# Kernel tuning notes

Hardware: AMD Instinct MI355X
Metric: run time of the kernel (lower is better)

Reference implementation:

```python
import jax, jax.numpy as jnp
import numpy as np

NUM_HEADS = 16
D_MODEL = 1024
D_K = 64
D_V = 64
NEG_INF = -1e9


def setup_inputs() -> dict:
    key = jax.random.key(0)
    ks = jax.random.split(key, 7)
    B, S = 2, 2048
    Q = jax.random.normal(ks[0], (B, S, D_MODEL), dtype=jnp.float32)
    K = jax.random.normal(ks[1], (B, S, D_MODEL), dtype=jnp.float32)
    V = jax.random.normal(ks[2], (B, S, D_MODEL), dtype=jnp.float32)
    s = 1.0 / np.sqrt(D_MODEL)
    W_q = jax.random.normal(ks[3], (D_MODEL, D_K * NUM_HEADS), dtype=jnp.float32) * s
    W_k = jax.random.normal(ks[4], (D_MODEL, D_K), dtype=jnp.float32) * s
    W_v = jax.random.normal(ks[5], (D_MODEL, D_V), dtype=jnp.float32) * s
    W_o = jax.random.normal(ks[6], (D_V * NUM_HEADS, D_MODEL), dtype=jnp.float32) * (1.0 / np.sqrt(D_V * NUM_HEADS))
    return {"Q": Q, "K": K, "V": V, "W_q": W_q, "W_k": W_k, "W_v": W_v, "W_o": W_o}


def reference(Q, K, V, W_q, W_k, W_v, W_o):
    B, Sq, _ = Q.shape
    Sk = K.shape[1]
    # projections: Q -> per-head, K/V -> single shared head (MQA)
    q = (Q @ W_q).reshape(B, Sq, NUM_HEADS, D_K).transpose(0, 2, 1, 3)  # [B,H,Sq,Dk]
    k = K @ W_k  # [B,Sk,Dk]
    v = V @ W_v  # [B,Sk,Dv]
    scores = jnp.einsum('bhqd,bkd->bhqk', q, k) / jnp.sqrt(jnp.float32(D_K))
    causal = jnp.tril(jnp.ones((Sq, Sk), dtype=bool))  # [Sq,Sk]
    scores = jnp.where(causal[None, None], scores, NEG_INF)
    attn = jax.nn.softmax(scores, axis=-1)  # [B,H,Sq,Sk]
    out = jnp.einsum('bhqk,bkd->bhqd', attn, v)  # [B,H,Sq,Dv]
    out = out.transpose(0, 2, 1, 3).reshape(B, Sq, NUM_HEADS * D_V)
    return out @ W_o
```

## Files before the change

### kernel.cpp

```cpp
#include <hip/hip_runtime.h>
#include <hip/hip_bf16.h>
#include <cstdint>

typedef __bf16 bf16_t;
typedef __bf16 bf16x8 __attribute__((ext_vector_type(8)));
typedef __bf16 bf16x4 __attribute__((ext_vector_type(4)));
typedef float  floatx4 __attribute__((ext_vector_type(4)));

__device__ __forceinline__ bf16_t f2bf(float x) { return (bf16_t)x; }

__device__ __forceinline__ void gll16(const void* g, void* l) {
  __builtin_amdgcn_global_load_lds((const __attribute__((address_space(1))) void*)g,
                                   (__attribute__((address_space(3))) void*)l, 16, 0, 0);
}

#define S_LEN 2048
#define NHEAD 16
#define NTILE 32

__global__ __launch_bounds__(256) void transpose_w2(const float* __restrict__ W0,
                                                    const float* __restrict__ W1,
                                                    bf16_t* __restrict__ O0,
                                                    bf16_t* __restrict__ O1,
                                                    int K, int N) {
  const float* W = blockIdx.z ? W1 : W0;
  bf16_t* Wt = blockIdx.z ? O1 : O0;
  __shared__ float tile[32][33];
  int n0 = blockIdx.x * 32, k0 = blockIdx.y * 32;
  int tx = threadIdx.x & 31, ty = threadIdx.x >> 5;
#pragma unroll
  for (int r = 0; r < 4; ++r)
    tile[ty + 8 * r][tx] = W[(size_t)(k0 + ty + 8 * r) * N + n0 + tx];
  __syncthreads();
#pragma unroll
  for (int r = 0; r < 4; ++r)
    Wt[(size_t)(n0 + ty + 8 * r) * K + k0 + tx] = f2bf(tile[tx][ty + 8 * r]);
}

template <int OUTMODE, bool A_FP32>
__global__ __launch_bounds__(256, 2) void gemm_async(const void* __restrict__ Ain,
                                                     const bf16_t* __restrict__ Bt,
                                                     void* __restrict__ Cout,
                                                     int M, int N, int K) {
  constexpr int BK = 64;
  __shared__ __align__(16) bf16_t As[64 * BK];
  __shared__ __align__(16) bf16_t Bs[128 * BK];
  const int tid = threadIdx.x;
  const int wave = tid >> 6, lane = tid & 63;
  const int quad = lane >> 4, lm = lane & 15;
  const int wr = wave >> 1, wc = wave & 1;
  const int m0 = blockIdx.x * 64, n0 = blockIdx.y * 128;

  floatx4 acc[2][4];
#pragma unroll
  for (int i = 0; i < 2; ++i)
#pragma unroll
    for (int j = 0; j < 4; ++j) acc[i][j] = (floatx4){0.f, 0.f, 0.f, 0.f};

  for (int k0 = 0; k0 < K; k0 += BK) {
    if constexpr (A_FP32) {
#pragma unroll
      for (int rd = 0; rd < 2; ++rd) {
        int idx = rd * 256 + tid, row = idx >> 3, ch = (idx & 7) ^ (row & 7);
        const float* src = (const float*)Ain + (size_t)(m0 + row) * K + k0 + ch * 8;
        float4 f0 = *(const float4*)src;
        float4 f1 = *(const float4*)(src + 4);
        bf16x8 o;
        o[0] = f2bf(f0.x); o[1] = f2bf(f0.y); o[2] = f2bf(f0.z); o[3] = f2bf(f0.w);
        o[4] = f2bf(f1.x); o[5] = f2bf(f1.y); o[6] = f2bf(f1.z); o[7] = f2bf(f1.w);
        *(bf16x8*)&As[idx * 8] = o;
      }
    } else {
#pragma unroll
      for (int rd = 0; rd < 2; ++rd) {
        int idx = rd * 256 + tid, row = idx >> 3, ch = (idx & 7) ^ (row & 7);
        gll16((const bf16_t*)Ain + (size_t)(m0 + row) * K + k0 + ch * 8,
              As + (rd * 256 + wave * 64) * 8);
      }
    }
#pragma unroll
    for (int rd = 0; rd < 4; ++rd) {
      int idx = rd * 256 + tid, row = idx >> 3, ch = (idx & 7) ^ (row & 7);
      gll16(Bt + (size_t)(n0 + row) * K + k0 + ch * 8,
            Bs + (rd * 256 + wave * 64) * 8);
    }
    __syncthreads();
    const int sw = lm & 7;
    bf16x8 af[2][2], bfr[4][2];
#pragma unroll
    for (int i = 0; i < 2; ++i) {
      const bf16_t* base = &As[(wr * 32 + i * 16 + lm) * BK];
      af[i][0] = *(const bf16x8*)(base + ((quad ^ sw) * 8));
      af[i][1] = *(const bf16x8*)(base + (((4 + quad) ^ sw) * 8));
    }
#pragma unroll
    for (int j = 0; j < 4; ++j) {
      const bf16_t* base = &Bs[(wc * 64 + j * 16 + lm) * BK];
      bfr[j][0] = *(const bf16x8*)(base + ((quad ^ sw) * 8));
      bfr[j][1] = *(const bf16x8*)(base + (((4 + quad) ^ sw) * 8));
    }
#pragma unroll
    for (int ks = 0; ks < 2; ++ks)
#pragma unroll
      for (int i = 0; i < 2; ++i)
#pragma unroll
        for (int j = 0; j < 4; ++j)
          acc[i][j] = __builtin_amdgcn_mfma_f32_16x16x32_bf16(af[i][ks], bfr[j][ks],
                                                              acc[i][j], 0, 0, 0);
    __syncthreads();
  }
#pragma unroll
  for (int i = 0; i < 2; ++i) {
#pragma unroll
    for (int j = 0; j < 4; ++j) {
      int row0 = m0 + wr * 32 + i * 16 + quad * 4;
      int col = n0 + wc * 64 + j * 16 + lm;
#pragma unroll
      for (int r = 0; r < 4; ++r) {
        if constexpr (OUTMODE == 3)
          ((bf16_t*)Cout)[(size_t)(row0 + r) * N + col] = f2bf(acc[i][j][r] * 0.125f);
        else
          ((float*)Cout)[(size_t)(row0 + r) * N + col] = acc[i][j][r];
      }
    }
  }
}

__global__ __launch_bounds__(256) void gemm_kv(const float* __restrict__ Kin,
                                               const float* __restrict__ Vin,
                                               const bf16_t* __restrict__ Wkt,
                                               const bf16_t* __restrict__ Wvt,
                                               bf16_t* __restrict__ kp,
                                               bf16_t* __restrict__ vpt,
                                               int M, int K) {
  constexpr int BK = 32, LDK = 40, N = 64;
  const int isV = blockIdx.z;
  const float* A32 = isV ? Vin : Kin;
  const bf16_t* Bt = isV ? Wvt : Wkt;
  __shared__ __align__(16) bf16_t As[64 * LDK];
  __shared__ __align__(16) bf16_t Bs[64 * LDK];
  const int tid = threadIdx.x;
  const int wave = tid >> 6, lane = tid & 63;
  const int quad = lane >> 4, lm = lane & 15;
  const int wr = wave >> 1, wc = wave & 1;
  const int m0 = blockIdx.x * 64;

  floatx4 acc[2][2];
#pragma unroll
  for (int i = 0; i < 2; ++i)
#pragma unroll
    for (int j = 0; j < 2; ++j) acc[i][j] = (floatx4){0.f, 0.f, 0.f, 0.f};

  for (int k0 = 0; k0 < K; k0 += BK) {
    {
      int row = tid >> 2, c8 = tid & 3;
      const float* src = A32 + (size_t)(m0 + row) * K + k0 + c8 * 8;
      float4 f0 = *(const float4*)src;
      float4 f1 = *(const float4*)(src + 4);
      bf16x8 o;
      o[0] = f2bf(f0.x); o[1] = f2bf(f0.y); o[2] = f2bf(f0.z); o[3] = f2bf(f0.w);
      o[4] = f2bf(f1.x); o[5] = f2bf(f1.y); o[6] = f2bf(f1.z); o[7] = f2bf(f1.w);
      *(bf16x8*)&As[row * LDK + c8 * 8] = o;
    }
    {
      int row = tid >> 2, c8 = tid & 3;
      *(bf16x8*)&Bs[row * LDK + c8 * 8] =
          *(const bf16x8*)(Bt + (size_t)row * K + k0 + c8 * 8);
    }
    __syncthreads();
    bf16x8 af[2], bfr[2];
#pragma unroll
    for (int i = 0; i < 2; ++i)
      af[i] = *(const bf16x8*)&As[(wr * 32 + i * 16 + lm) * LDK + quad * 8];
#pragma unroll
    for (int j = 0; j < 2; ++j)
      bfr[j] = *(const bf16x8*)&Bs[(wc * 32 + j * 16 + lm) * LDK + quad * 8];
#pragma unroll
    for (int i = 0; i < 2; ++i)
#pragma unroll
      for (int j = 0; j < 2; ++j)
        acc[i][j] = __builtin_amdgcn_mfma_f32_16x16x32_bf16(af[i], bfr[j],
                                                            acc[i][j], 0, 0, 0);
    __syncthreads();
  }
#pragma unroll
  for (int i = 0; i < 2; ++i) {
#pragma unroll
    for (int j = 0; j < 2; ++j) {
      int row0 = m0 + wr * 32 + i * 16 + quad * 4;
      int col = wc * 32 + j * 16 + lm;
      if (isV) {
        bf16x4 o;
#pragma unroll
        for (int r = 0; r < 4; ++r) o[r] = f2bf(acc[i][j][r]);
        *(bf16x4*)&vpt[(size_t)col * M + row0] = o;
      } else {
#pragma unroll
        for (int r = 0; r < 4; ++r)
          kp[(size_t)(row0 + r) * N + col] = f2bf(acc[i][j][r]);
      }
    }
  }
}

__global__ __launch_bounds__(256, 4) void flash_mqa(const bf16_t* __restrict__ q,
                                                    const bf16_t* __restrict__ kk,
                                                    const bf16_t* __restrict__ vt,
                                                    bf16_t* __restrict__ O,
                                                    int BStot) {
  const int qt = NTILE - 1 - blockIdx.x;
  const int h = blockIdx.y, b = blockIdx.z;
  const int tid = threadIdx.x;
  const int wave = tid >> 6, lane = tid & 63;
  const int quad = lane >> 4, lm = lane & 15;

  __shared__ __align__(16) bf16_t k_lds[2][64 * 64];
  __shared__ __align__(16) bf16_t vt_lds[2][64 * 64];
  __shared__ __align__(16) bf16_t p_lds[4][16 * 64];

  const size_t bS = (size_t)b * S_LEN;
  const int qb = qt * 64;

  bf16x8 qf[2];
  {
    const bf16_t* qp = q + (bS + qb + wave * 16 + lm) * 1024 + h * 64;
    qf[0] = *(const bf16x8*)(qp + quad * 8);
    qf[1] = *(const bf16x8*)(qp + 32 + quad * 8);
  }
  bf16x8 onesf;
#pragma unroll
  for (int j = 0; j < 8; ++j) onesf[j] = f2bf(1.0f);

  floatx4 acc[4];
  floatx4 ps = (floatx4){0.f, 0.f, 0.f, 0.f};
#pragma unroll
  for (int t = 0; t < 4; ++t) acc[t] = (floatx4){0.f, 0.f, 0.f, 0.f};

  const int srow = tid >> 3, sc8 = tid & 7;
  const int swst = (sc8 ^ (srow & 7)) * 8;
  bf16x8 kst[2], vst[2];
  auto load_kv = [&](int kt) {
    const int k0 = kt * 64;
#pragma unroll
    for (int it = 0; it < 2; ++it) {
      int r = it * 32 + srow;
      kst[it] = *(const bf16x8*)(kk + (bS + k0 + r) * 64 + sc8 * 8);
      vst[it] = *(const bf16x8*)(vt + (size_t)r * BStot + bS + k0 + sc8 * 8);
    }
  };
  auto write_kv = [&](int buf) {
#pragma unroll
    for (int it = 0; it < 2; ++it) {
      int r = it * 32 + srow;
      *(bf16x8*)&k_lds[buf][r * 64 + swst] = kst[it];
      *(bf16x8*)&vt_lds[buf][r * 64 + swst] = vst[it];
    }
  };

  load_kv(0);
  write_kv(0);
  __syncthreads();

  const int sw = lm & 7;
  const int qloc = wave * 16 + lm;

  for (int kt = 0; kt <= qt; ++kt) {
    const int cur = kt & 1;
    if (kt < qt) load_kv(kt + 1);

    floatx4 s[4];
#pragma unroll
    for (int t = 0; t < 4; ++t) {
      const bf16_t* kb = &k_lds[cur][(t * 16 + lm) * 64];
      bf16x8 a0 = *(const bf16x8*)(kb + ((quad ^ sw) * 8));
      bf16x8 a1 = *(const bf16x8*)(kb + (((4 + quad) ^ sw) * 8));
      floatx4 cc = (floatx4){0.f, 0.f, 0.f, 0.f};
      cc = __builtin_amdgcn_mfma_f32_16x16x32_bf16(a0, qf[0], cc, 0, 0, 0);
      cc = __builtin_amdgcn_mfma_f32_16x16x32_bf16(a1, qf[1], cc, 0, 0, 0);
      s[t] = cc;
    }
    if (kt == qt) {
#pragma unroll
      for (int t = 0; t < 4; ++t)
#pragma unroll
        for (int r = 0; r < 4; ++r) {
          int kj = t * 16 + quad * 4 + r;
          s[t][r] = (kj <= qloc) ? __expf(s[t][r]) : 0.f;
        }
    } else {
#pragma unroll
      for (int t = 0; t < 4; ++t)
#pragma unroll
        for (int r = 0; r < 4; ++r) s[t][r] = __expf(s[t][r]);
    }
#pragma unroll
    for (int t = 0; t < 4; ++t) {
      bf16x4 pk;
#pragma unroll
      for (int r = 0; r < 4; ++r) pk[r] = f2bf(s[t][r]);
      *(bf16x4*)&p_lds[wave][lm * 64 + (((2 * t + (quad >> 1)) ^ sw) * 8) + (quad & 1) * 4] = pk;
    }
    bf16x8 p0 = *(const bf16x8*)&p_lds[wave][lm * 64 + ((quad ^ sw) * 8)];
    bf16x8 p1 = *(const bf16x8*)&p_lds[wave][lm * 64 + (((4 + quad) ^ sw) * 8)];
    ps = __builtin_amdgcn_mfma_f32_16x16x32_bf16(p0, onesf, ps, 0, 0, 0);
    ps = __builtin_amdgcn_mfma_f32_16x16x32_bf16(p1, onesf, ps, 0, 0, 0);
#pragma unroll
    for (int t = 0; t < 4; ++t) {
      const bf16_t* vb = &vt_lds[cur][(t * 16 + lm) * 64];
      bf16x8 v0 = *(const bf16x8*)(vb + ((quad ^ sw) * 8));
      bf16x8 v1 = *(const bf16x8*)(vb + (((4 + quad) ^ sw) * 8));
      acc[t] = __builtin_amdgcn_mfma_f32_16x16x32_bf16(p0, v0, acc[t], 0, 0, 0);
      acc[t] = __builtin_amdgcn_mfma_f32_16x16x32_bf16(p1, v1, acc[t], 0, 0, 0);
    }
    if (kt < qt) write_kv(1 - cur);
    __syncthreads();
  }

  float rl[4];
#pragma unroll
  for (int r = 0; r < 4; ++r) rl[r] = 1.0f / ps[r];
  const int q0 = qb + wave * 16 + quad * 4;
#pragma unroll
  for (int t = 0; t < 4; ++t)
#pragma unroll
    for (int r = 0; r < 4; ++r)
      O[(bS + q0 + r) * 1024 + h * 64 + t * 16 + lm] = f2bf(acc[t][r] * rl[r]);
}

extern "C" void kernel_launch(void* const* d_in, const int* in_sizes, int n_in,
                              void* d_out, int out_size, void* d_ws, size_t ws_size,
                              hipStream_t stream) {
  const float* Q  = (const float*)d_in[0];
  const float* K  = (const float*)d_in[1];
  const float* V  = (const float*)d_in[2];
  const float* Wq = (const float*)d_in[3];
  const float* Wk = (const float*)d_in[4];
  const float* Wv = (const float*)d_in[5];
  const float* Wo = (const float*)d_in[6];

  const int BS = in_sizes[0] / 1024;
  const int B  = BS / S_LEN;

  bf16_t* ws  = (bf16_t*)d_ws;
  bf16_t* qp  = ws;
  bf16_t* Ob  = qp  + (size_t)BS * 1024;
  bf16_t* Wqt = Ob  + (size_t)BS * 1024;
  bf16_t* Wot = Wqt + (size_t)1024 * 1024;
  bf16_t* Wkt = Wot + (size_t)1024 * 1024;
  bf16_t* Wvt = Wkt + (size_t)64 * 1024;
  bf16_t* kp  = Wvt + (size_t)64 * 1024;
  bf16_t* vpt = kp  + (size_t)BS * 64;

  transpose_w2<<<dim3(32, 32, 2), 256, 0, stream>>>(Wq, Wo, Wqt, Wot, 1024, 1024);
  transpose_w2<<<dim3(2, 32, 2),  256, 0, stream>>>(Wk, Wv, Wkt, Wvt, 1024, 64);

  gemm_kv<<<dim3(BS / 64, 1, 2), 256, 0, stream>>>(K, V, Wkt, Wvt, kp, vpt, BS, 1024);

  gemm_async<3, true><<<dim3(BS / 64, 8), 256, 0, stream>>>(Q, Wqt, qp, BS, 1024, 1024);

  flash_mqa<<<dim3(NTILE, NHEAD, B), 256, 0, stream>>>(qp, kp, vpt, Ob, BS);

  gemm_async<0, false><<<dim3(BS / 64, 8), 256, 0, stream>>>(Ob, Wot, (float*)d_out, BS, 1024, 1024);
}
```

Measured before the change: 216.5 us.

## Restructure MQA attention so each wave owns a head and all 64 query rows

The flash attention kernel changes from four waves each handling 16 query rows of one head to two waves per block, each handling all 64 query rows of its own head. The shared K/V tile in LDS is reused across two heads per block, and each K/V fragment read from LDS feeds four MFMA row-tiles instead of one. This halves the number of blocks and cuts global and LDS traffic for K/V per head. In exchange it raises per-thread register use (16 accumulator tiles plus 8 Q fragments), lowers occupancy via launch bounds of (128,2), and leaves fewer waves to hide latency.

```diff
diff --git a/kernel.cpp b/kernel.cpp
--- a/kernel.cpp
+++ b/kernel.cpp
@@ -203,57 +203,64 @@
   }
 }
 
-__global__ __launch_bounds__(256, 4) void flash_mqa(const bf16_t* __restrict__ q,
+__global__ __launch_bounds__(128, 2) void flash_mqa(const bf16_t* __restrict__ q,
                                                     const bf16_t* __restrict__ kk,
                                                     const bf16_t* __restrict__ vt,
                                                     bf16_t* __restrict__ O,
                                                     int BStot) {
   const int qt = NTILE - 1 - blockIdx.x;
-  const int h = blockIdx.y, b = blockIdx.z;
+  const int hb = blockIdx.y, b = blockIdx.z;
   const int tid = threadIdx.x;
   const int wave = tid >> 6, lane = tid & 63;
   const int quad = lane >> 4, lm = lane & 15;
+  const int h = hb * 2 + wave;
 
   __shared__ __align__(16) bf16_t k_lds[2][64 * 64];
-  __shared__ __align__(16) bf16_t vt_lds[2][64 * 64];
-  __shared__ __align__(16) bf16_t p_lds[4][16 * 64];
+  __shared__ __align__(16) bf16_t v_lds[2][64 * 64];
+  __shared__ __align__(16) bf16_t p_lds[2][64 * 64];
 
   const size_t bS = (size_t)b * S_LEN;
   const int qb = qt * 64;
-
-  bf16x8 qf[2];
-  {
-    const bf16_t* qp = q + (bS + qb + wave * 16 + lm) * 1024 + h * 64;
-    qf[0] = *(const bf16x8*)(qp + quad * 8);
-    qf[1] = *(const bf16x8*)(qp + 32 + quad * 8);
+  const int sw = lm & 7;
+
+  bf16x8 qf[4][2];
+#pragma unroll
+  for (int m = 0; m < 4; ++m) {
+    const bf16_t* qp = q + (bS + qb + m * 16 + lm) * 1024 + h * 64;
+    qf[m][0] = *(const bf16x8*)(qp + quad * 8);
+    qf[m][1] = *(const bf16x8*)(qp + 32 + quad * 8);
   }
   bf16x8 onesf;
 #pragma unroll
   for (int j = 0; j < 8; ++j) onesf[j] = f2bf(1.0f);
 
-  floatx4 acc[4];
-  floatx4 ps = (floatx4){0.f, 0.f, 0.f, 0.f};
-#pragma unroll
-  for (int t = 0; t < 4; ++t) acc[t] = (floatx4){0.f, 0.f, 0.f, 0.f};
-
-  const int srow = tid >> 3, sc8 = tid & 7;
-  const int swst = (sc8 ^ (srow & 7)) * 8;
-  bf16x8 kst[2], vst[2];
+  floatx4 acc[4][4];
+  floatx4 ps[4];
+#pragma unroll
+  for (int m = 0; m < 4; ++m) {
+    ps[m] = (floatx4){0.f, 0.f, 0.f, 0.f};
+#pragma unroll
+    for (int t = 0; t < 4; ++t) acc[m][t] = (floatx4){0.f, 0.f, 0.f, 0.f};
+  }
+
+  const int stid = tid;
+  bf16x8 kst[4], vst[4];
   auto load_kv = [&](int kt) {
     const int k0 = kt * 64;
 #pragma unroll
-    for (int it = 0; it < 2; ++it) {
-      int r = it * 32 + srow;
-      kst[it] = *(const bf16x8*)(kk + (bS + k0 + r) * 64 + sc8 * 8);
-      vst[it] = *(const bf16x8*)(vt + (size_t)r * BStot + bS + k0 + sc8 * 8);
+    for (int it = 0; it < 4; ++it) {
+      int idx = it * 128 + stid, r = idx >> 3, c8 = idx & 7;
+      kst[it] = *(const bf16x8*)(kk + (bS + k0 + r) * 64 + c8 * 8);
+      vst[it] = *(const bf16x8*)(vt + (size_t)r * BStot + bS + k0 + c8 * 8);
     }
   };
   auto write_kv = [&](int buf) {
 #pragma unroll
-    for (int it = 0; it < 2; ++it) {
-      int r = it * 32 + srow;
-      *(bf16x8*)&k_lds[buf][r * 64 + swst] = kst[it];
-      *(bf16x8*)&vt_lds[buf][r * 64 + swst] = vst[it];
+    for (int it = 0; it < 4; ++it) {
+      int idx = it * 128 + stid, r = idx >> 3, c8 = idx & 7;
+      int addr = r * 64 + ((c8 ^ (r & 7)) * 8);
+      *(bf16x8*)&k_lds[buf][addr] = kst[it];
+      *(bf16x8*)&v_lds[buf][addr] = vst[it];
     }
   };
 
@@ -261,70 +268,85 @@
   write_kv(0);
   __syncthreads();
 
-  const int sw = lm & 7;
-  const int qloc = wave * 16 + lm;
-
   for (int kt = 0; kt <= qt; ++kt) {
     const int cur = kt & 1;
     if (kt < qt) load_kv(kt + 1);
 
-    floatx4 s[4];
+    const bool diag = (kt == qt);
 #pragma unroll
     for (int t = 0; t < 4; ++t) {
       const bf16_t* kb = &k_lds[cur][(t * 16 + lm) * 64];
       bf16x8 a0 = *(const bf16x8*)(kb + ((quad ^ sw) * 8));
       bf16x8 a1 = *(const bf16x8*)(kb + (((4 + quad) ^ sw) * 8));
-      floatx4 cc = (floatx4){0.f, 0.f, 0.f, 0.f};
-      cc = __builtin_amdgcn_mfma_f32_16x16x32_bf16(a0, qf[0], cc, 0, 0, 0);
-      cc = __builtin_amdgcn_mfma_f32_16x16x32_bf16(a1, qf[1], cc, 0, 0, 0);
-      s[t] = cc;
-    }
-    if (kt == qt) {
-#pragma unroll
-      for (int t = 0; t < 4; ++t)
-#pragma unroll
-        for (int r = 0; r < 4; ++r) {
-          int kj = t * 16 + quad * 4 + r;
-          s[t][r] = (kj <= qloc) ? __expf(s[t][r]) : 0.f;
+      floatx4 s[4];
+#pragma unroll
+      for (int m = 0; m < 4; ++m) {
+        floatx4 cc = (floatx4){0.f, 0.f, 0.f, 0.f};
+        cc = __builtin_amdgcn_mfma_f32_16x16x32_bf16(a0, qf[m][0], cc, 0, 0, 0);
+        cc = __builtin_amdgcn_mfma_f32_16x16x32_bf16(a1, qf[m][1], cc, 0, 0, 0);
+        s[m] = cc;
+      }
+      if (diag) {
+#pragma unroll
+        for (int m = 0; m < 4; ++m) {
+          int qq = m * 16 + lm;
+#pragma unroll
+          for (int r = 0; r < 4; ++r) {
+            int kj = t * 16 + quad * 4 + r;
+            s[m][r] = (kj <= qq) ? __expf(s[m][r]) : 0.f;
+          }
         }
-    } else {
-#pragma unroll
-      for (int t = 0; t < 4; ++t)
-#pragma unroll
-        for (int r = 0; r < 4; ++r) s[t][r] = __expf(s[t][r]);
+      } else {
+#pragma unroll
+        for (int m = 0; m < 4; ++m)
+#pragma unroll
+          for (int r = 0; r < 4; ++r) s[m][r] = __expf(s[m][r]);
+      }
+#pragma unroll
+      for (int m = 0; m < 4; ++m) {
+        bf16x4 pk;
+#pragma unroll
+        for (int r = 0; r < 4; ++r) pk[r] = f2bf(s[m][r]);
+        *(bf16x4*)&p_lds[wave][(m * 16 + lm) * 64 +
+                               (((2 * t + (quad >> 1)) ^ sw) * 8) + (quad & 1) * 4] = pk;
+      }
+    }
+    bf16x8 p0[4], p1[4];
+#pragma unroll
+    for (int m = 0; m < 4; ++m) {
+      const bf16_t* pb = &p_lds[wave][(m * 16 + lm) * 64];
+      p0[m] = *(const bf16x8*)(pb + ((quad ^ sw) * 8));
+      p1[m] = *(const bf16x8*)(pb + (((4 + quad) ^ sw) * 8));
+      ps[m] = __builtin_amdgcn_mfma_f32_16x16x32_bf16(p0[m], onesf, ps[m], 0, 0, 0);
+      ps[m] = __builtin_amdgcn_mfma_f32_16x16x32_bf16(p1[m], onesf, ps[m], 0, 0, 0);
     }
 #pragma unroll
     for (int t = 0; t < 4; ++t) {
-      bf16x4 pk;
-#pragma unroll
-      for (int r = 0; r < 4; ++r) pk[r] = f2bf(s[t][r]);
-      *(bf16x4*)&p_lds[wave][lm * 64 + (((2 * t + (quad >> 1)) ^ sw) * 8) + (quad & 1) * 4] = pk;
-    }
-    bf16x8 p0 = *(const bf16x8*)&p_lds[wave][lm * 64 + ((quad ^ sw) * 8)];
-    bf16x8 p1 = *(const bf16x8*)&p_lds[wave][lm * 64 + (((4 + quad) ^ sw) * 8)];
-    ps = __builtin_amdgcn_mfma_f32_16x16x32_bf16(p0, onesf, ps, 0, 0, 0);
-    ps = __builtin_amdgcn_mfma_f32_16x16x32_bf16(p1, onesf, ps, 0, 0, 0);
-#pragma unroll
-    for (int t = 0; t < 4; ++t) {
-      const bf16_t* vb = &vt_lds[cur][(t * 16 + lm) * 64];
+      const bf16_t* vb = &v_lds[cur][(t * 16 + lm) * 64];
       bf16x8 v0 = *(const bf16x8*)(vb + ((quad ^ sw) * 8));
       bf16x8 v1 = *(const bf16x8*)(vb + (((4 + quad) ^ sw) * 8));
-      acc[t] = __builtin_amdgcn_mfma_f32_16x16x32_bf16(p0, v0, acc[t], 0, 0, 0);
-      acc[t] = __builtin_amdgcn_mfma_f32_16x16x32_bf16(p1, v1, acc[t], 0, 0, 0);
+#pragma unroll
+      for (int m = 0; m < 4; ++m) {
+        acc[m][t] = __builtin_amdgcn_mfma_f32_16x16x32_bf16(p0[m], v0, acc[m][t], 0, 0, 0);
+        acc[m][t] = __builtin_amdgcn_mfma_f32_16x16x32_bf16(p1[m], v1, acc[m][t], 0, 0, 0);
+      }
     }
     if (kt < qt) write_kv(1 - cur);
     __syncthreads();
   }
 
-  float rl[4];
-#pragma unroll
-  for (int r = 0; r < 4; ++r) rl[r] = 1.0f / ps[r];
-  const int q0 = qb + wave * 16 + quad * 4;
-#pragma unroll
-  for (int t = 0; t < 4; ++t)
-#pragma unroll
-    for (int r = 0; r < 4; ++r)
-      O[(bS + q0 + r) * 1024 + h * 64 + t * 16 + lm] = f2bf(acc[t][r] * rl[r]);
+#pragma unroll
+  for (int m = 0; m < 4; ++m) {
+    float rl[4];
+#pragma unroll
+    for (int r = 0; r < 4; ++r) rl[r] = 1.0f / ps[m][r];
+    const int q0 = qb + m * 16 + quad * 4;
+#pragma unroll
+    for (int t = 0; t < 4; ++t)
+#pragma unroll
+      for (int r = 0; r < 4; ++r)
+        O[(bS + q0 + r) * 1024 + h * 64 + t * 16 + lm] = f2bf(acc[m][t][r] * rl[r]);
+  }
 }
 
 extern "C" void kernel_launch(void* const* d_in, const int* in_sizes, int n_in,
@@ -358,7 +380,7 @@
 
   gemm_async<3, true><<<dim3(BS / 64, 8), 256, 0, stream>>>(Q, Wqt, qp, BS, 1024, 1024);
 
-  flash_mqa<<<dim3(NTILE, NHEAD, B), 256, 0, stream>>>(qp, kp, vpt, Ob, BS);
+  flash_mqa<<<dim3(NTILE, NHEAD / 2, B), 128, 0, stream>>>(qp, kp, vpt, Ob, BS);
 
   gemm_async<0, false><<<dim3(BS / 64, 8), 256, 0, stream>>>(Ob, Wot, (float*)d_out, BS, 1024, 1024);
 }
```

Measured after the change: 236.6 us. 9.3% more time.
